# Kernel tuning notes

Hardware: AMD Instinct MI355X
Metric: run time of the kernel (lower is better)

Reference implementation:

```python
import jax, jax.numpy as jnp
import numpy as np

B, T, H, V = 32, 256, 512, 50000
R, CELL, N_CELLS = 4, 64, 64
CLIP = 50000.0
EPS = 1e-6
XI = R*CELL + R + CELL + 1 + CELL + CELL + R + 1 + 1 + 3*R  # 471


def setup_inputs() -> dict:
    key = jax.random.key(0)
    ks = jax.random.split(key, 8)
    s = 0.05
    return {
        "source": jax.random.randint(ks[0], (B, T), 0, V),
        "source_lengths": jax.random.randint(ks[1], (B,), 1, T),
        "emb_table": jax.random.normal(ks[2], (V, H), jnp.float32) * s,
        "Wih": jax.random.normal(ks[3], (H + R*CELL, 4*H), jnp.float32) * s,
        "Whh": jax.random.normal(ks[4], (H, 4*H), jnp.float32) * s,
        "b_lstm": jnp.zeros((4*H,), jnp.float32),
        "W_xi": jax.random.normal(ks[5], (H, XI), jnp.float32) * s,
        "b_xi": jnp.zeros((XI,), jnp.float32),
        "W_out": jax.random.normal(ks[6], (H + R*CELL, H), jnp.float32) * s,
        "b_out": jnp.zeros((H,), jnp.float32),
    }


def _content_w(M, keys, beta):
    # cosine-similarity content addressing; M:[B,N,W], keys:[B,K,W] -> [B,K,N]
    Mn = M / (jnp.linalg.norm(M, axis=-1, keepdims=True) + EPS)
    kn = keys / (jnp.linalg.norm(keys, axis=-1, keepdims=True) + EPS)
    sim = jnp.einsum('bnw,bkw->bkn', Mn, kn)
    return jax.nn.softmax(sim * beta[..., None], axis=-1)


def _dnc(emb_table, Wih, Whh, b_lstm, W_xi, b_xi, W_out, b_out, source):
    Bq = source.shape[0]
    x = emb_table[source]  # [B,T,H] embedding lookup

    def step(state, x_t):
        h, c, M, u, p, L, wr, ww, r = state
        # LSTM controller: input = [emb_t ; flattened read vectors]
        inp = jnp.concatenate([x_t, r.reshape(Bq, R*CELL)], -1)
        gates = inp @ Wih + h @ Whh + b_lstm
        gi, gf, gg, go = jnp.split(gates, 4, axis=-1)
        c = jax.nn.sigmoid(gf)*c + jax.nn.sigmoid(gi)*jnp.tanh(gg)
        h = jax.nn.sigmoid(go)*jnp.tanh(c)
        # interface vector
        xi = h @ W_xi + b_xi
        o = [0]
        def take(n):
            out = xi[:, o[0]:o[0]+n]; o[0] += n; return out
        read_keys = take(R*CELL).reshape(Bq, R, CELL)
        beta_r = 1.0 + jax.nn.softplus(take(R))              # [B,R]
        write_key = take(CELL)                                # [B,W]
        beta_w = 1.0 + jax.nn.softplus(take(1))              # [B,1]
        erase = jax.nn.sigmoid(take(CELL))                    # [B,W]
        write_vec = take(CELL)                                # [B,W]
        free = jax.nn.sigmoid(take(R))                        # [B,R]
        g_a = jax.nn.sigmoid(take(1))                         # [B,1]
        g_w = jax.nn.sigmoid(take(1))                         # [B,1]
        pi = jax.nn.softmax(take(3*R).reshape(Bq, R, 3), -1)  # read modes
        # write content weighting
        cw_w = _content_w(M, write_key[:, None, :], beta_w)[:, 0]  # [B,N]
        # usage / retention
        psi = jnp.prod(1.0 - free[:, :, None] * wr, axis=1)   # [B,N]
        u = (u + ww - u * ww) * psi
        # allocation weighting (sort-based)
        idx = jnp.argsort(u, axis=-1)
        su = jnp.take_along_axis(u, idx, axis=-1)
        prod_excl = jnp.concatenate(
            [jnp.ones((Bq, 1), u.dtype), jnp.cumprod(su, -1)[:, :-1]], -1)
        a = jnp.zeros_like(u).at[jnp.arange(Bq)[:, None], idx].set((1.0 - su) * prod_excl)
        ww = g_w * (g_a * a + (1.0 - g_a) * cw_w)             # [B,N]
        # memory write (erase then add)
        M = M * (1.0 - ww[:, :, None] * erase[:, None, :]) + ww[:, :, None] * write_vec[:, None, :]
        # temporal link matrix + precedence
        L = (1.0 - ww[:, :, None] - ww[:, None, :]) * L + ww[:, :, None] * p[:, None, :]
        L = L * (1.0 - jnp.eye(N_CELLS, dtype=L.dtype))
        p = (1.0 - ww.sum(-1, keepdims=True)) * p + ww
        # read weights: backward / content / forward modes
        fwd_w = jnp.einsum('bnm,brm->brn', L, wr)
        bwd_w = jnp.einsum('bmn,brm->brn', L, wr)
        cw_r = _content_w(M, read_keys, beta_r)
        wr = pi[..., 0:1]*bwd_w + pi[..., 1:2]*cw_r + pi[..., 2:3]*fwd_w
        r = jnp.einsum('brn,bnw->brw', wr, M)                 # read vectors
        y = jnp.concatenate([h, r.reshape(Bq, R*CELL)], -1) @ W_out + b_out
        y = jnp.clip(y, -CLIP, CLIP)  # clip=vocab_size in source
        return (h, c, M, u, p, L, wr, ww, r), y

    z, d = jnp.zeros, x.dtype
    init = (z((Bq, H), d), z((Bq, H), d), z((Bq, N_CELLS, CELL), d),
            z((Bq, N_CELLS), d), z((Bq, N_CELLS), d), z((Bq, N_CELLS, N_CELLS), d),
            z((Bq, R, N_CELLS), d), z((Bq, N_CELLS), d), z((Bq, R, CELL), d))
    _, ys = jax.lax.scan(step, init, jnp.swapaxes(x, 0, 1))
    return jnp.swapaxes(ys, 0, 1)  # [B,T,H]


def reference(source, source_lengths, emb_table, Wih, Whh, b_lstm, W_xi, b_xi, W_out, b_out):
    del source_lengths  # present in signature but unused by the original forward
    return _dnc(emb_table, Wih, Whh, b_lstm, W_xi, b_xi, W_out, b_out, source)
```

## Files before the change

kernel.cpp:

```cpp
#include <hip/hip_runtime.h>


constexpr int NBLK = 128;
constexpr int BS   = 256;
constexpr int BQ   = 32;
constexpr int TT   = 256;
constexpr int HH   = 512;
constexpr int RH   = 4;
constexpr int NC   = 64;
constexpr int XI   = 471;
constexpr int KG   = 1280;
constexpr int KGP  = 1288;
constexpr int WOP  = 776;
constexpr float CLIPV = 50000.0f;
constexpr float EPSV  = 1e-6f;

typedef __bf16 bf16x8 __attribute__((ext_vector_type(8)));
typedef float  f32x4  __attribute__((ext_vector_type(4)));
typedef unsigned long long u64;

constexpr int OFF_WG   = 0;
constexpr int OFF_WO   = OFF_WG  + 16*KGP*2;
constexpr int OFF_GT   = OFF_WO  + 16*WOP*2;
constexpr int OFF_CST  = OFF_GT  + 32*17*4;
constexpr int OFF_HLB  = OFF_CST + 512;
constexpr int OFF_DNC  = OFF_HLB + 1024;
constexpr int D_M    = 0;
constexpr int D_L    = D_M   + 64*65*4;
constexpr int D_XIR  = D_L   + 64*65*4;
constexpr int D_WR   = D_XIR + 480*4;
constexpr int D_FWD  = D_WR  + 256*4;
constexpr int D_BWD  = D_FWD + 256*4;
constexpr int D_SIMR = D_BWD + 256*4;
constexpr int D_VEC  = D_SIMR+ 256*4;
constexpr int D_SCAL = D_VEC + 8*64*4;
constexpr int SMEM_BYTES = OFF_DNC + D_SCAL + 32*4;

constexpr size_t WS_HFLG  = 0;
constexpr size_t WS_XDONE = 128;
constexpr size_t WS_RFLG  = 8192;
constexpr size_t WS_HBUF  = 8192 + 2048;
constexpr size_t WS_RBUF  = WS_HBUF + 65536;
constexpr size_t WS_WXBT  = WS_RBUF + 16384;
constexpr size_t WS_EMB   = WS_WXBT + 491520;
constexpr size_t WS_MIN   = WS_WXBT + 491520;
constexpr size_t WS_FULL  = WS_EMB + 8388608;
constexpr size_t WS_XIB   = WS_FULL;
constexpr size_t XIB_BYTES = 32ull * 512 * 4;
constexpr size_t WS_FULL2 = WS_XIB + XIB_BYTES;
constexpr size_t WS_ZERO  = WS_RBUF + 16384;

__device__ __forceinline__ unsigned short f2b(float f) {
  unsigned u = __builtin_bit_cast(unsigned, f);
  u += 0x7fffu + ((u >> 16) & 1u);
  return (unsigned short)(u >> 16);
}
__device__ __forceinline__ float sigf(float x) { return 1.0f / (1.0f + expf(-x)); }
__device__ __forceinline__ float softplusf(float x) { return (x > 20.0f) ? x : log1pf(expf(x)); }
__device__ __forceinline__ float wsum(float v) {
  #pragma unroll
  for (int o = 32; o; o >>= 1) v += __shfl_xor(v, o, 64);
  return v;
}
__device__ __forceinline__ float wmaxr(float v) {
  #pragma unroll
  for (int o = 32; o; o >>= 1) v = fmaxf(v, __shfl_xor(v, o, 64));
  return v;
}
__device__ __forceinline__ f32x4 mfma16(bf16x8 a, bf16x8 b, f32x4 c) {
  return __builtin_amdgcn_mfma_f32_16x16x32_bf16(a, b, c, 0, 0, 0);
}
__device__ __forceinline__ void drain_vm() {
  asm volatile("s_waitcnt vmcnt(0)" ::: "memory");
}

__device__ __forceinline__ void st_u64(u64* p, u64 v) {
  __hip_atomic_store(p, v, __ATOMIC_RELAXED, __HIP_MEMORY_SCOPE_AGENT);
}
__device__ __forceinline__ u64 ld_u64(const u64* p) {
  return __hip_atomic_load(p, __ATOMIC_RELAXED, __HIP_MEMORY_SCOPE_AGENT);
}
__device__ __forceinline__ unsigned ld_flag(const unsigned* p) {
  return __hip_atomic_load(p, __ATOMIC_RELAXED, __HIP_MEMORY_SCOPE_AGENT);
}
__device__ __forceinline__ void add_flag(unsigned* p) {
  __hip_atomic_fetch_add(p, 1u, __ATOMIC_RELAXED, __HIP_MEMORY_SCOPE_AGENT);
}
struct alignas(16) U64x2 { u64 a, b; };
__device__ __forceinline__ bf16x8 ld_bf16x8_mall(const unsigned short* p) {
  U64x2 v;
  v.a = ld_u64((const u64*)p);
  v.b = ld_u64((const u64*)p + 1);
  return __builtin_bit_cast(bf16x8, v);
}

__device__ __forceinline__ void wait_cnt(const unsigned* cnt, unsigned target) {
  if ((threadIdx.x >> 6) == 0) {
    while (ld_flag(cnt) < target) {  }
  }
  __builtin_amdgcn_fence(__ATOMIC_ACQUIRE, "workgroup");
  __syncthreads();
}

__global__ __launch_bounds__(BS, 1) void dnc_kernel(
    const int* __restrict__ src, const float* __restrict__ emb,
    const float* __restrict__ Wih, const float* __restrict__ Whh,
    const float* __restrict__ b_lstm, const float* __restrict__ W_xi,
    const float* __restrict__ b_xi, const float* __restrict__ W_out,
    const float* __restrict__ b_out, float* __restrict__ out,
    unsigned* __restrict__ hdone, unsigned* __restrict__ rdone,
    unsigned* __restrict__ xdone,
    unsigned short* __restrict__ hbuf, unsigned short* __restrict__ rbuf,
    unsigned short* __restrict__ wxbT_, unsigned short* __restrict__ embbuf_,
    float* __restrict__ xibuf)
{
  extern __shared__ char smem[];
  __bf16* lWg  = (__bf16*)(smem + OFF_WG);
  __bf16* lWo  = (__bf16*)(smem + OFF_WO);
  float*  gt   = (float*)(smem + OFF_GT);
  float*  cst  = (float*)(smem + OFF_CST);
  __bf16* hlb  = (__bf16*)(smem + OFF_HLB);
  char*   dnc  = smem + OFF_DNC;
  float* Ml   = (float*)(dnc + D_M);
  float* Ll   = (float*)(dnc + D_L);
  float* xir  = (float*)(dnc + D_XIR);
  float* wrl  = (float*)(dnc + D_WR);
  float* fwd  = (float*)(dnc + D_FWD);
  float* bwd  = (float*)(dnc + D_BWD);
  float* simr = (float*)(dnc + D_SIMR);
  float* uu   = (float*)(dnc + D_VEC);
  float* pp   = uu + 64;
  float* wwl  = uu + 128;
  float* aas  = uu + 192;
  float* nrmo = uu + 256;
  float* nrmn = uu + 320;
  float* simw = uu + 384;
  float* er   = uu + 448;
  float* scal = (float*)(dnc + D_SCAL);

  const int tid  = threadIdx.x;
  const int blk  = blockIdx.x;
  const int lane = tid & 63;
  const int wv   = tid >> 6;
  const int q    = lane >> 4;
  const int n16  = lane & 15;
  const int j0   = blk << 2;
  const __bf16* wxbT = (const __bf16*)wxbT_;
  const __bf16* embbuf = (const __bf16*)embbuf_;
  const bool is_dnc = (blk < BQ);
  const bool is_y   = (blk >= 64 && blk < 96);
  const bool is_xi  = (blk >= 96 && blk < 126) && (xibuf != nullptr) && (wxbT_ != nullptr);

  for (int e = tid; e < 16 * KG; e += BS) {
    int k = e >> 4, cc = e & 15;
    int gcol = ((cc >> 2) << 9) + j0 + (cc & 3);
    float w = (k < 768) ? Wih[k * 2048 + gcol] : Whh[(k - 768) * 2048 + gcol];
    lWg[cc * KGP + k] = (__bf16)w;
  }
  if (is_y) {
    for (int e = tid; e < 16 * 768; e += BS) {
      int k = e >> 4, cc = e & 15;
      int col = ((blk - 64) << 4) + cc;
      lWo[cc * WOP + k] = (__bf16)W_out[k * HH + col];
    }
  }
  if (wxbT_) {
    for (int w = blk * BS + tid; w < 61440; w += NBLK * BS) {
      int e = w << 2;
      int jb    = e & 7;
      int lane_ = (e >> 3) & 63;
      int f     = e >> 9;
      int col   = (f >> 4) * 16 + (lane_ & 15);
      int k0    = (f & 15) * 32 + (lane_ >> 4) * 8 + jb;
      u64 pk = 0;
      if (col < XI) {
        #pragma unroll
        for (int j = 0; j < 4; ++j) {
          unsigned short us = f2b(W_xi[(size_t)(k0 + j) * XI + col]);
          pk |= (u64)us << (16 * j);
        }
      }
      st_u64((u64*)wxbT_ + w, pk);
    }
  }
  if (embbuf_) {
    for (int rr = blk * 2 + (tid >> 7); rr < BQ * TT; rr += NBLK * 2) {
      const int t128 = tid & 127;
      const float* s = emb + (size_t)src[rr] * HH;
      float4 v = *(const float4*)(s + t128 * 4);
      u64 pk = (u64)f2b(v.x) | ((u64)f2b(v.y) << 16)
             | ((u64)f2b(v.z) << 32) | ((u64)f2b(v.w) << 48);
      st_u64((u64*)(embbuf_ + (size_t)rr * HH + t128 * 4), pk);
    }
  }
  if (tid < 128) cst[tid] = 0.0f;
  if (is_dnc) {
    for (int e = tid; e < 64 * 65; e += BS) { Ml[e] = 0.0f; Ll[e] = 0.0f; }
    if (tid < 64) { uu[tid] = 0.0f; pp[tid] = 0.0f; wwl[tid] = 0.0f; }
    wrl[tid] = 0.0f;
  }
  __syncthreads();
  if (tid == 0) add_flag(hdone);

  f32x4 ax0 = {0.f, 0.f, 0.f, 0.f}, ax1 = {0.f, 0.f, 0.f, 0.f};
  const int bb = ((wv & 1) << 4) + n16;

  auto x_mfmas = [&](int tt) {
    const __bf16* eb = embbuf ? (embbuf + ((size_t)bb * TT + tt) * HH) : nullptr;
    const float* ep = embbuf ? nullptr
                             : (emb + (size_t)src[bb * TT + tt] * HH + (q << 3));
    #pragma unroll
    for (int ks = 0; ks < 16; ++ks) {
      const int kq = (ks << 5) + (q << 3);
      bf16x8 A;
      if (eb) {
        A = *(const bf16x8*)(eb + kq);
      } else {
        const float* p = ep + (ks << 5);
        #pragma unroll
        for (int j = 0; j < 8; ++j) A[j] = (__bf16)p[j];
      }
      bf16x8 Bf = *(const bf16x8*)(lWg + n16 * KGP + kq);
      if (ks & 1) ax1 = mfma16(A, Bf, ax1); else ax0 = mfma16(A, Bf, ax0);
    }
  };
  auto h_mfmas = [&](int slot) {
    const unsigned short* hp = hbuf + slot * (BQ * HH);
    #pragma unroll
    for (int ks = 16; ks < 32; ++ks) {
      const int off = ((ks - 16) << 5) + (q << 3);
      bf16x8 A = ld_bf16x8_mall(hp + bb * HH + off);
      bf16x8 Bf = *(const bf16x8*)(lWg + n16 * KGP + 768 + off);
      if (ks & 1) ax1 = mfma16(A, Bf, ax1); else ax0 = mfma16(A, Bf, ax0);
    }
  };
  auto r_mfmas = [&]() {
    #pragma unroll
    for (int ks = 32; ks < 40; ++ks) {
      const int off = ((ks - 32) << 5) + (q << 3);
      bf16x8 A = ld_bf16x8_mall(rbuf + bb * (RH * NC) + off);
      bf16x8 Bf = *(const bf16x8*)(lWg + n16 * KGP + 512 + off);
      if (ks & 1) ax1 = mfma16(A, Bf, ax1); else ax0 = mfma16(A, Bf, ax0);
    }
    const int gcol = ((n16 >> 2) << 9) + j0 + (n16 & 3);
    const float bias = b_lstm[gcol];
    #pragma unroll
    for (int j = 0; j < 4; ++j)
      gt[(((wv & 1) << 4) + (q << 2) + j) * 17 + n16] = ax0[j] + ax1[j] + bias;
  };
  auto do_y = [&](int t) {
    const unsigned short* hp = hbuf + ((t + 1) & 1) * (BQ * HH);
    const int mt = wv - 2;
    const int bby = (mt << 4) + n16;
    f32x4 a0 = {0.f, 0.f, 0.f, 0.f}, a1 = {0.f, 0.f, 0.f, 0.f};
    #pragma unroll
    for (int ks = 0; ks < 24; ++ks) {
      const int kq = (ks << 5) + (q << 3);
      bf16x8 A = (ks < 16) ? ld_bf16x8_mall(hp + bby * HH + kq)
                           : ld_bf16x8_mall(rbuf + bby * (RH * NC) + (kq - 512));
      bf16x8 Bf = *(const bf16x8*)(lWo + n16 * WOP + kq);
      if (ks & 1) a1 = mfma16(A, Bf, a1); else a0 = mfma16(A, Bf, a0);
    }
    const int col = ((blk - 64) << 4) + n16;
    const float bias = b_out[col];
    #pragma unroll
    for (int j = 0; j < 4; ++j) {
      int row = (mt << 4) + (q << 2) + j;
      float y = a0[j] + a1[j] + bias;
      y = fminf(fmaxf(y, -CLIPV), CLIPV);
      out[(size_t)row * (TT * HH) + (size_t)(t - 1) * HH + col] = y;
    }
  };
  auto do_xi = [&](int t) {
    const unsigned short* hp = hbuf + (t & 1) * (BQ * HH)
                             + (size_t)((((wv - 2) << 4) + n16) * HH) + (q << 3);
    const int ct = blk - 96;
    f32x4 acc = {0.f, 0.f, 0.f, 0.f};
    bf16x8 A[8];
    #pragma unroll
    for (int kt = 0; kt < 8; ++kt) A[kt] = ld_bf16x8_mall(hp + (kt << 5));
    #pragma unroll
    for (int kt = 0; kt < 8; ++kt) {
      bf16x8 Bf = *(const bf16x8*)(wxbT + (((size_t)(ct << 4) + kt) << 9) + (lane << 3));
      acc = mfma16(A[kt], Bf, acc);
    }
    #pragma unroll
    for (int kt = 0; kt < 8; ++kt) A[kt] = ld_bf16x8_mall(hp + ((8 + kt) << 5));
    #pragma unroll
    for (int kt = 0; kt < 8; ++kt) {
      bf16x8 Bf = *(const bf16x8*)(wxbT + (((size_t)(ct << 4) + 8 + kt) << 9) + (lane << 3));
      acc = mfma16(A[kt], Bf, acc);
    }
    const int col = (ct << 4) + n16;
    const float bias = b_xi[col];
    #pragma unroll
    for (int j = 0; j < 4; ++j) {
      float v = acc[j] + bias;
      unsigned lo = __builtin_bit_cast(unsigned, v);
      unsigned hi = __shfl_down(lo, 1, 64);
      if (!(n16 & 1)) {
        int batch = ((wv - 2) << 4) + (q << 2) + j;
        st_u64((u64*)(xibuf + ((size_t)batch << 9) + col),
               (u64)lo | ((u64)hi << 32));
      }
    }
    drain_vm();
    if (lane == 0) add_flag(xdone);
  };

  wait_cnt(hdone, 128u);
  if (wv < 2) x_mfmas(0);

  for (int t = 0; t < TT; ++t) {
    unsigned short* hcur = hbuf + (t & 1) * (BQ * HH);

    if (t > 0) wait_cnt(rdone, 32u * (unsigned)t);
    if (wv < 2) {
      r_mfmas();
    } else if (is_y && t > 0) {
      do_y(t);
    }
    __syncthreads();
    if (tid < BQ) {
      const int b = tid;
      u64 hv = 0;
      #pragma unroll
      for (int i = 0; i < 4; ++i) {
        float g_i = gt[b * 17 + i],     g_f = gt[b * 17 + 4 + i];
        float g_g = gt[b * 17 + 8 + i], g_o = gt[b * 17 + 12 + i];
        float c = cst[b * 4 + i];
        c = sigf(g_f) * c + sigf(g_i) * tanhf(g_g);
        float h = sigf(g_o) * tanhf(c);
        cst[b * 4 + i] = c;
        hv |= (u64)f2b(h) << (16 * i);
      }
      st_u64((u64*)(hcur + b * HH + j0), hv);
    }
    __syncthreads();
    if (tid == 0) add_flag(hdone);

    if (!is_dnc) {
      if (is_xi) {
        wait_cnt(hdone, 128u * (unsigned)(t + 2));
        if (wv >= 2) {
          do_xi(t);
        } else if (t < TT - 1) {
          ax0 = f32x4{0.f, 0.f, 0.f, 0.f};
          ax1 = f32x4{0.f, 0.f, 0.f, 0.f};
          x_mfmas(t + 1);
          h_mfmas(t & 1);
        }
      } else {
        if (wv < 2 && t < TT - 1) {
          ax0 = f32x4{0.f, 0.f, 0.f, 0.f};
          ax1 = f32x4{0.f, 0.f, 0.f, 0.f};
          x_mfmas(t + 1);
        }
        wait_cnt(hdone, 128u * (unsigned)(t + 2));
        if (wv < 2 && t < TT - 1) h_mfmas(t & 1);
      }
      continue;
    }

    if (xibuf && wxbT_) {
      wait_cnt(xdone, 60u * (unsigned)(t + 1));
      if (tid < 240) {
        u64 v = ld_u64((const u64*)(xibuf + ((size_t)blk << 9)) + tid);
        xir[tid * 2]     = __builtin_bit_cast(float, (unsigned)v);
        xir[tid * 2 + 1] = __builtin_bit_cast(float, (unsigned)(v >> 32));
      }
      __syncthreads();
    } else {
      wait_cnt(hdone, 128u * (unsigned)(t + 2));
      if (tid < 128) {
        u64 hv = ld_u64((const u64*)(hcur + blk * HH + tid * 4));
        #pragma unroll
        for (int i = 0; i < 4; ++i)
          hlb[tid * 4 + i] = __builtin_bit_cast(__bf16, (unsigned short)(hv >> (16 * i)));
      }
      __syncthreads();
      {
        constexpr int TPW = 8;
        f32x4 acc[TPW];
        #pragma unroll
        for (int i = 0; i < TPW; ++i) acc[i] = f32x4{0.f, 0.f, 0.f, 0.f};
        const int ct0 = wv * TPW;
        const int ntile = (ct0 + TPW <= 30) ? TPW : (30 - ct0);
        for (int kt = 0; kt < 16; ++kt) {
          bf16x8 Bf = {};
          if (n16 == 0) Bf = *(const bf16x8*)(hlb + kt * 32 + (q << 3));
          if (wxbT) {
            #pragma unroll
            for (int i = 0; i < TPW; ++i) {
              if (i < ntile) {
                const __bf16* ap = wxbT
                    + (((size_t)(ct0 + i) * 16 + kt) << 9) + (lane << 3);
                acc[i] = mfma16(*(const bf16x8*)ap, Bf, acc[i]);
              }
            }
          } else {
            #pragma unroll
            for (int i = 0; i < TPW; ++i) {
              if (i < ntile) {
                const int col = (ct0 + i) * 16 + n16;
                bf16x8 Af;
                #pragma unroll
                for (int j = 0; j < 8; ++j)
                  Af[j] = (col < XI) ? (__bf16)W_xi[(size_t)(kt * 32 + (q << 3) + j) * XI + col]
                                     : (__bf16)0.0f;
                acc[i] = mfma16(Af, Bf, acc[i]);
              }
            }
          }
        }
        if (n16 == 0) {
          const int rowb = (lane >> 4) * 4;
          #pragma unroll
          for (int i = 0; i < TPW; ++i) {
            if (i < ntile) {
              #pragma unroll
              for (int j = 0; j < 4; ++j) {
                int col = (ct0 + i) * 16 + rowb + j;
                if (col < XI) xir[col] = acc[i][j] + b_xi[col];
              }
            }
          }
        }
      }
      __syncthreads();
    }
    if (tid == 0) {
      scal[0] = 1.0f + softplusf(xir[324]);
      scal[1] = sigf(xir[457]);
      scal[2] = sigf(xir[458]);
    }
    if (tid >= 4 && tid < 8) {
      int r = tid - 4;
      scal[4 + r]  = 1.0f + softplusf(xir[256 + r]);
      scal[12 + r] = sigf(xir[453 + r]);
      float p0 = xir[459 + r * 3], p1 = xir[460 + r * 3], p2 = xir[461 + r * 3];
      float m = fmaxf(p0, fmaxf(p1, p2));
      float e0 = expf(p0 - m), e1 = expf(p1 - m), e2 = expf(p2 - m);
      float s = e0 + e1 + e2;
      scal[16 + r * 3 + 0] = e0 / s;
      scal[16 + r * 3 + 1] = e1 / s;
      scal[16 + r * 3 + 2] = e2 / s;
    }
    if (tid >= 64 && tid < 128) er[tid - 64] = sigf(xir[325 + (tid - 64)]);
    __syncthreads();
    if (wv == 0) {
      float s = 0.f;
      for (int w = 0; w < 64; ++w) { float m = Ml[lane * 65 + w]; s += m * m; }
      nrmo[lane] = sqrtf(s) + EPSV;
    } else if (wv == 1) {
      float d = 0.f;
      for (int w = 0; w < 64; ++w) d += Ml[lane * 65 + w] * xir[260 + w];
      simw[lane] = d;
      float v = xir[260 + lane];
      float s2 = wsum(v * v);
      if (lane == 0) scal[3] = sqrtf(s2) + EPSV;
    } else if (wv == 2) {
      float psi = 1.f;
      #pragma unroll
      for (int r = 0; r < 4; ++r) psi *= (1.f - scal[12 + r] * wrl[r * 64 + lane]);
      float un = uu[lane], w_ = wwl[lane];
      un = (un + w_ - un * w_) * psi;
      uu[lane] = un;
      float v = un; int id = lane;
      for (int k = 2; k <= 64; k <<= 1) {
        for (int j2 = k >> 1; j2 > 0; j2 >>= 1) {
          float ov = __shfl_xor(v, j2, 64);
          int   oi = __shfl_xor(id, j2, 64);
          bool up    = ((lane & k) == 0);
          bool lower = ((lane & j2) == 0);
          bool lt = (v < ov) || (v == ov && id < oi);
          bool keep = (lower == up) ? lt : !lt;
          if (!keep) { v = ov; id = oi; }
        }
      }
      float cp = v;
      for (int d2 = 1; d2 < 64; d2 <<= 1) {
        float o = __shfl_up(cp, d2, 64);
        if (lane >= d2) cp *= o;
      }
      float pe = __shfl_up(cp, 1, 64);
      if (lane == 0) pe = 1.0f;
      aas[id] = (1.0f - v) * pe;
    }
    __syncthreads();
    if (wv == 0) {
      float x = simw[lane] / (nrmo[lane] * scal[3]) * scal[0];
      float mx = wmaxr(x);
      float e = expf(x - mx);
      float s = wsum(e);
      float cw = e / s;
      wwl[lane] = scal[2] * (scal[1] * aas[lane] + (1.f - scal[1]) * cw);
    }
    __syncthreads();
    {
      const int n = tid >> 2, c4 = (tid & 3) << 4;
      float wwn = wwl[n];
      #pragma unroll
      for (int w = 0; w < 16; ++w) {
        int wj = c4 + w;
        Ml[n * 65 + wj] = Ml[n * 65 + wj] * (1.f - wwn * er[wj]) + wwn * xir[389 + wj];
      }
      #pragma unroll
      for (int w = 0; w < 16; ++w) {
        int m2 = c4 + w;
        float Lv = (n == m2) ? 0.f
                 : ((1.f - wwn - wwl[m2]) * Ll[n * 65 + m2] + wwn * pp[m2]);
        Ll[n * 65 + m2] = Lv;
      }
    }
    __syncthreads();
    {
      float f = 0.f, bw2 = 0.f, d = 0.f;
      for (int m2 = 0; m2 < 64; ++m2) {
        float wrm = wrl[wv * 64 + m2];
        f   += Ll[lane * 65 + m2] * wrm;
        bw2 += Ll[m2 * 65 + lane] * wrm;
      }
      fwd[wv * 64 + lane] = f;
      bwd[wv * 64 + lane] = bw2;
      for (int w = 0; w < 64; ++w) d += Ml[lane * 65 + w] * xir[wv * 64 + w];
      simr[wv * 64 + lane] = d;
      float v = xir[wv * 64 + lane];
      float s2 = wsum(v * v);
      if (lane == 0) scal[8 + wv] = sqrtf(s2) + EPSV;
      if (wv == 0) {
        float s = 0.f;
        for (int w = 0; w < 64; ++w) { float m = Ml[lane * 65 + w]; s += m * m; }
        nrmn[lane] = sqrtf(s) + EPSV;
      }
    }
    __syncthreads();
    {
      float x = simr[wv * 64 + lane] / (nrmn[lane] * scal[8 + wv]) * scal[4 + wv];
      float mx = wmaxr(x);
      float e = expf(x - mx);
      float s = wsum(e);
      float cw = e / s;
      float wrn = scal[16 + wv * 3 + 0] * bwd[wv * 64 + lane]
                + scal[16 + wv * 3 + 1] * cw
                + scal[16 + wv * 3 + 2] * fwd[wv * 64 + lane];
      wrl[wv * 64 + lane] = wrn;
      if (wv == 3) {
        float s3 = wsum(wwl[lane]);
        pp[lane] = (1.f - s3) * pp[lane] + wwl[lane];
      }
    }
    __syncthreads();
    {
      float rv = 0.f;
      for (int n2 = 0; n2 < 64; ++n2) rv += wrl[wv * 64 + n2] * Ml[n2 * 65 + lane];
      unsigned v0 = f2b(rv);
      unsigned v1 = __shfl_down(v0, 1, 64);
      unsigned v2 = __shfl_down(v0, 2, 64);
      unsigned v3 = __shfl_down(v0, 3, 64);
      if ((lane & 3) == 0) {
        u64 pk = (u64)v0 | ((u64)v1 << 16) | ((u64)v2 << 32) | ((u64)v3 << 48);
        st_u64((u64*)(rbuf + blk * (RH * NC) + wv * 64 + lane), pk);
      }
    }
    __syncthreads();
    if (tid == 0) add_flag(rdone);
    if (wv < 2 && t < TT - 1) {
      ax0 = f32x4{0.f, 0.f, 0.f, 0.f};
      ax1 = f32x4{0.f, 0.f, 0.f, 0.f};
      x_mfmas(t + 1);
      h_mfmas(t & 1);
    }
  }

  if (is_y) {
    wait_cnt(rdone, 32u * (unsigned)TT);
    if (wv >= 2) do_y(TT);
  }
}

extern "C" void kernel_launch(void* const* d_in, const int* in_sizes, int n_in,
                              void* d_out, int out_size, void* d_ws, size_t ws_size,
                              hipStream_t stream) {
  const int*   src    = (const int*)d_in[0];
  const float* emb    = (const float*)d_in[2];
  const float* Wih    = (const float*)d_in[3];
  const float* Whh    = (const float*)d_in[4];
  const float* b_lstm = (const float*)d_in[5];
  const float* W_xi   = (const float*)d_in[6];
  const float* b_xi   = (const float*)d_in[7];
  const float* W_out  = (const float*)d_in[8];
  const float* b_out  = (const float*)d_in[9];
  float* out = (float*)d_out;

  char* ws = (char*)d_ws;
  unsigned*       hdone  = (unsigned*)(ws + WS_HFLG);
  unsigned*       xdone  = (unsigned*)(ws + WS_XDONE);
  unsigned*       rdone  = (unsigned*)(ws + WS_RFLG);
  unsigned short* hbuf   = (unsigned short*)(ws + WS_HBUF);
  unsigned short* rbuf   = (unsigned short*)(ws + WS_RBUF);
  unsigned short* wxbT   = (ws_size >= WS_MIN)   ? (unsigned short*)(ws + WS_WXBT) : nullptr;
  unsigned short* embbuf = (ws_size >= WS_FULL)  ? (unsigned short*)(ws + WS_EMB)  : nullptr;
  float*          xibuf  = (ws_size >= WS_FULL2) ? (float*)(ws + WS_XIB)           : nullptr;

  hipMemsetAsync(d_ws, 0, WS_ZERO, stream);
  hipFuncSetAttribute((const void*)dnc_kernel,
                      hipFuncAttributeMaxDynamicSharedMemorySize, SMEM_BYTES);
  dnc_kernel<<<dim3(NBLK), dim3(BS), SMEM_BYTES, stream>>>(
      src, emb, Wih, Whh, b_lstm, W_xi, b_xi, W_out, b_out, out,
      hdone, rdone, xdone, hbuf, rbuf, wxbT, embbuf, xibuf);
}
```

Baseline: 7.946 ms.

## Tag xi buffer entries with timestep to replace counter-flag sync; reuse memory norms

```diff
diff --git a/kernel.cpp b/kernel.cpp
--- a/kernel.cpp
+++ b/kernel.cpp
@@ -46,8 +46,9 @@
 constexpr size_t WS_MIN   = WS_WXBT + 491520;
 constexpr size_t WS_FULL  = WS_EMB + 8388608;
 constexpr size_t WS_XIB   = WS_FULL;
-constexpr size_t XIB_BYTES = 32ull * 512 * 4;
-constexpr size_t WS_FULL2 = WS_XIB + XIB_BYTES;
+constexpr size_t WS_FULL2 = WS_XIB + 32ull * 512 * 4;
+constexpr size_t XIBT_BYTES = 32ull * 512 * 8;
+constexpr size_t WS_FULL3 = WS_XIB + XIBT_BYTES;
 constexpr size_t WS_ZERO  = WS_RBUF + 16384;
 
 __device__ __forceinline__ unsigned short f2b(float f) {
@@ -112,7 +113,7 @@
     unsigned* __restrict__ xdone,
     unsigned short* __restrict__ hbuf, unsigned short* __restrict__ rbuf,
     unsigned short* __restrict__ wxbT_, unsigned short* __restrict__ embbuf_,
-    float* __restrict__ xibuf)
+    float* __restrict__ xibF, u64* __restrict__ xibT)
 {
   extern __shared__ char smem[];
   __bf16* lWg  = (__bf16*)(smem + OFF_WG);
@@ -132,8 +133,8 @@
   float* pp   = uu + 64;
   float* wwl  = uu + 128;
   float* aas  = uu + 192;
-  float* nrmo = uu + 256;
-  float* nrmn = uu + 320;
+  float* nb0  = uu + 256;
+  float* nb1  = uu + 320;
   float* simw = uu + 384;
   float* er   = uu + 448;
   float* scal = (float*)(dnc + D_SCAL);
@@ -149,7 +150,7 @@
   const __bf16* embbuf = (const __bf16*)embbuf_;
   const bool is_dnc = (blk < BQ);
   const bool is_y   = (blk >= 64 && blk < 96);
-  const bool is_xi  = (blk >= 96 && blk < 126) && (xibuf != nullptr) && (wxbT_ != nullptr);
+  const bool is_xi  = (blk >= 96 && blk < 126) && (xibF || xibT) && (wxbT_ != nullptr);
 
   for (int e = tid; e < 16 * KG; e += BS) {
     int k = e >> 4, cc = e & 15;
@@ -196,7 +197,7 @@
   if (tid < 128) cst[tid] = 0.0f;
   if (is_dnc) {
     for (int e = tid; e < 64 * 65; e += BS) { Ml[e] = 0.0f; Ll[e] = 0.0f; }
-    if (tid < 64) { uu[tid] = 0.0f; pp[tid] = 0.0f; wwl[tid] = 0.0f; }
+    if (tid < 64) { uu[tid] = 0.0f; pp[tid] = 0.0f; wwl[tid] = 0.0f; nb0[tid] = EPSV; }
     wrl[tid] = 0.0f;
   }
   __syncthreads();
@@ -292,20 +293,30 @@
       acc = mfma16(A[kt], Bf, acc);
     }
     const int col = (ct << 4) + n16;
-    const float bias = b_xi[col];
-    #pragma unroll
-    for (int j = 0; j < 4; ++j) {
-      float v = acc[j] + bias;
-      unsigned lo = __builtin_bit_cast(unsigned, v);
-      unsigned hi = __shfl_down(lo, 1, 64);
-      if (!(n16 & 1)) {
+    const float bias = (col < XI) ? b_xi[col] : 0.0f;
+    if (xibT) {
+      #pragma unroll
+      for (int j = 0; j < 4; ++j) {
+        float v = acc[j] + bias;
         int batch = ((wv - 2) << 4) + (q << 2) + j;
-        st_u64((u64*)(xibuf + ((size_t)batch << 9) + col),
-               (u64)lo | ((u64)hi << 32));
-      }
-    }
-    drain_vm();
-    if (lane == 0) add_flag(xdone);
+        st_u64(xibT + ((size_t)batch << 9) + col,
+               (u64)__builtin_bit_cast(unsigned, v) | ((u64)(unsigned)(t + 1) << 32));
+      }
+    } else {
+      #pragma unroll
+      for (int j = 0; j < 4; ++j) {
+        float v = acc[j] + bias;
+        unsigned lo = __builtin_bit_cast(unsigned, v);
+        unsigned hi = __shfl_down(lo, 1, 64);
+        if (!(n16 & 1)) {
+          int batch = ((wv - 2) << 4) + (q << 2) + j;
+          st_u64((u64*)(xibF + ((size_t)batch << 9) + col),
+                 (u64)lo | ((u64)hi << 32));
+        }
+      }
+      drain_vm();
+      if (lane == 0) add_flag(xdone);
+    }
   };
 
   wait_cnt(hdone, 128u);
@@ -362,10 +373,23 @@
       continue;
     }
 
-    if (xibuf && wxbT_) {
+    if (xibT && wxbT_) {
+      const u64* xb = xibT + ((size_t)blk << 9);
+      const unsigned tg = (unsigned)(t + 1);
+      u64 v1 = 0, v2 = 0;
+      bool o1 = false, o2 = (tid >= 224);
+      for (;;) {
+        if (!o1) { v1 = ld_u64(xb + tid);       o1 = ((unsigned)(v1 >> 32) == tg); }
+        if (!o2) { v2 = ld_u64(xb + 256 + tid); o2 = ((unsigned)(v2 >> 32) == tg); }
+        if (o1 && o2) break;
+      }
+      xir[tid] = __builtin_bit_cast(float, (unsigned)v1);
+      if (tid < 224) xir[256 + tid] = __builtin_bit_cast(float, (unsigned)v2);
+      __syncthreads();
+    } else if (xibF && wxbT_) {
       wait_cnt(xdone, 60u * (unsigned)(t + 1));
       if (tid < 240) {
-        u64 v = ld_u64((const u64*)(xibuf + ((size_t)blk << 9)) + tid);
+        u64 v = ld_u64((const u64*)(xibF + ((size_t)blk << 9)) + tid);
         xir[tid * 2]     = __builtin_bit_cast(float, (unsigned)v);
         xir[tid * 2 + 1] = __builtin_bit_cast(float, (unsigned)(v >> 32));
       }
@@ -429,30 +453,9 @@
       }
       __syncthreads();
     }
-    if (tid == 0) {
-      scal[0] = 1.0f + softplusf(xir[324]);
-      scal[1] = sigf(xir[457]);
-      scal[2] = sigf(xir[458]);
-    }
-    if (tid >= 4 && tid < 8) {
-      int r = tid - 4;
-      scal[4 + r]  = 1.0f + softplusf(xir[256 + r]);
-      scal[12 + r] = sigf(xir[453 + r]);
-      float p0 = xir[459 + r * 3], p1 = xir[460 + r * 3], p2 = xir[461 + r * 3];
-      float m = fmaxf(p0, fmaxf(p1, p2));
-      float e0 = expf(p0 - m), e1 = expf(p1 - m), e2 = expf(p2 - m);
-      float s = e0 + e1 + e2;
-      scal[16 + r * 3 + 0] = e0 / s;
-      scal[16 + r * 3 + 1] = e1 / s;
-      scal[16 + r * 3 + 2] = e2 / s;
-    }
-    if (tid >= 64 && tid < 128) er[tid - 64] = sigf(xir[325 + (tid - 64)]);
-    __syncthreads();
-    if (wv == 0) {
-      float s = 0.f;
-      for (int w = 0; w < 64; ++w) { float m = Ml[lane * 65 + w]; s += m * m; }
-      nrmo[lane] = sqrtf(s) + EPSV;
-    } else if (wv == 1) {
+    const float* nbR = (t & 1) ? nb1 : nb0;
+    float*       nbW = (t & 1) ? nb0 : nb1;
+    if (wv == 1) {
       float d = 0.f;
       for (int w = 0; w < 64; ++w) d += Ml[lane * 65 + w] * xir[260 + w];
       simw[lane] = d;
@@ -460,9 +463,10 @@
       float s2 = wsum(v * v);
       if (lane == 0) scal[3] = sqrtf(s2) + EPSV;
     } else if (wv == 2) {
-      float psi = 1.f;
-      #pragma unroll
-      for (int r = 0; r < 4; ++r) psi *= (1.f - scal[12 + r] * wrl[r * 64 + lane]);
+      float fr0 = sigf(xir[453]), fr1 = sigf(xir[454]);
+      float fr2 = sigf(xir[455]), fr3 = sigf(xir[456]);
+      float psi = (1.f - fr0 * wrl[lane]) * (1.f - fr1 * wrl[64 + lane])
+                * (1.f - fr2 * wrl[128 + lane]) * (1.f - fr3 * wrl[192 + lane]);
       float un = uu[lane], w_ = wwl[lane];
       un = (un + w_ - un * w_) * psi;
       uu[lane] = un;
@@ -486,10 +490,28 @@
       float pe = __shfl_up(cp, 1, 64);
       if (lane == 0) pe = 1.0f;
       aas[id] = (1.0f - v) * pe;
+    } else if (wv == 3) {
+      if (lane == 0) {
+        scal[0] = 1.0f + softplusf(xir[324]);
+        scal[1] = sigf(xir[457]);
+        scal[2] = sigf(xir[458]);
+      }
+      if (lane >= 4 && lane < 8) {
+        int r = lane - 4;
+        scal[4 + r] = 1.0f + softplusf(xir[256 + r]);
+        float p0 = xir[459 + r * 3], p1 = xir[460 + r * 3], p2 = xir[461 + r * 3];
+        float m = fmaxf(p0, fmaxf(p1, p2));
+        float e0 = expf(p0 - m), e1 = expf(p1 - m), e2 = expf(p2 - m);
+        float s = e0 + e1 + e2;
+        scal[16 + r * 3 + 0] = e0 / s;
+        scal[16 + r * 3 + 1] = e1 / s;
+        scal[16 + r * 3 + 2] = e2 / s;
+      }
+      er[lane] = sigf(xir[325 + lane]);
     }
     __syncthreads();
     if (wv == 0) {
-      float x = simw[lane] / (nrmo[lane] * scal[3]) * scal[0];
+      float x = simw[lane] / (nbR[lane] * scal[3]) * scal[0];
       float mx = wmaxr(x);
       float e = expf(x - mx);
       float s = wsum(e);
@@ -531,12 +553,12 @@
       if (wv == 0) {
         float s = 0.f;
         for (int w = 0; w < 64; ++w) { float m = Ml[lane * 65 + w]; s += m * m; }
-        nrmn[lane] = sqrtf(s) + EPSV;
+        nbW[lane] = sqrtf(s) + EPSV;
       }
     }
     __syncthreads();
     {
-      float x = simr[wv * 64 + lane] / (nrmn[lane] * scal[8 + wv]) * scal[4 + wv];
+      float x = simr[wv * 64 + lane] / (nbW[lane] * scal[8 + wv]) * scal[4 + wv];
       float mx = wmaxr(x);
       float e = expf(x - mx);
       float s = wsum(e);
@@ -601,12 +623,16 @@
   unsigned short* rbuf   = (unsigned short*)(ws + WS_RBUF);
   unsigned short* wxbT   = (ws_size >= WS_MIN)   ? (unsigned short*)(ws + WS_WXBT) : nullptr;
   unsigned short* embbuf = (ws_size >= WS_FULL)  ? (unsigned short*)(ws + WS_EMB)  : nullptr;
-  float*          xibuf  = (ws_size >= WS_FULL2) ? (float*)(ws + WS_XIB)           : nullptr;
+  const bool tagged      = (ws_size >= WS_FULL3);
+  u64*   xibT  = tagged ? (u64*)(ws + WS_XIB) : nullptr;
+  float* xibF  = (!tagged && ws_size >= WS_FULL2) ? (float*)(ws + WS_XIB) : nullptr;
 
   hipMemsetAsync(d_ws, 0, WS_ZERO, stream);
+  if (tagged)
+    hipMemsetAsync(ws + WS_XIB, 0, XIBT_BYTES, stream);
   hipFuncSetAttribute((const void*)dnc_kernel,
                       hipFuncAttributeMaxDynamicSharedMemorySize, SMEM_BYTES);
   dnc_kernel<<<dim3(NBLK), dim3(BS), SMEM_BYTES, stream>>>(
       src, emb, Wih, Whh, b_lstm, W_xi, b_xi, W_out, b_out, out,
-      hdone, rdone, xdone, hbuf, rbuf, wxbT, embbuf, xibuf);
-}
+      hdone, rdone, xdone, hbuf, rbuf, wxbT, embbuf, xibF, xibT);
+}
```

New measurement: 6.995 ms. 12.0% less time.
